# Kernel tuning notes

Measured on AMD Instinct MI355X. Metric: run time of the kernel, lower is better.

Reference implementation:

```python
import jax, jax.numpy as jnp
import numpy as np

H = 8          # num heads
DK = 64        # d_model // H
D_MODEL = 512
WIN = 256


def setup_inputs() -> dict:
    key = jax.random.key(0)
    ks = jax.random.split(key, 12)
    B, S = 2, 2048
    mk = lambda k, shape, s=1.0: jax.random.normal(k, shape, dtype=jnp.float32) * s
    inp = {
        "query": mk(ks[0], (B, S, D_MODEL)),
        "key_in": mk(ks[1], (B, S, D_MODEL)),
        "value": mk(ks[2], (B, S, D_MODEL)),
        # nn.Linear(d_model, d_model) weights (out,in) and biases, x4
        "Wq": mk(ks[3], (D_MODEL, D_MODEL), 0.02), "bq": jnp.zeros((D_MODEL,), jnp.float32),
        "Wk": mk(ks[4], (D_MODEL, D_MODEL), 0.02), "bk": jnp.zeros((D_MODEL,), jnp.float32),
        "Wv": mk(ks[5], (D_MODEL, D_MODEL), 0.02), "bv": jnp.zeros((D_MODEL,), jnp.float32),
        "Wo": mk(ks[6], (D_MODEL, D_MODEL), 0.02), "bo": jnp.zeros((D_MODEL,), jnp.float32),
    }
    return inp


def reference(query, key_in, value, Wq, bq, Wk, bk, Wv, bv, Wo, bo):
    B, S, D = query.shape
    scale = np.float32(1.0 / np.sqrt(DK))

    def proj(x, W, b):
        # (B,S,D) -> (B,H,S,DK)
        return (x @ W.T + b).reshape(B, S, H, DK).transpose(0, 2, 1, 3)

    q = proj(query, Wq, bq)
    k = proj(key_in, Wk, bk)
    v = proj(value, Wv, bv)

    # Faithful to naive_masked_matmul: full (B,H,S,S) scores, with entries
    # OUTSIDE the sliding window left at exactly 0.0 (NOT -inf) before softmax.
    scores = jnp.einsum('bhid,bhjd->bhij', q, k) * scale
    idx = jnp.arange(S)
    band = jnp.abs(idx[:, None] - idx[None, :]) <= (WIN // 2)  # (S,S) bool
    scores = jnp.where(band, scores, jnp.float32(0.0))

    p_attn = jax.nn.softmax(scores, axis=-1)
    x = jnp.einsum('bhij,bhjd->bhid', p_attn, v)          # (B,H,S,DK)
    x = x.transpose(0, 2, 1, 3).reshape(B, S, D)          # (B,S,D)
    return x @ Wo.T + bo
```

## Files before the change

kernel.cpp:

```cpp
#include <hip/hip_runtime.h>
#include <hip/hip_bf16.h>

#define SS 2048
#define DD 512
#define HWIN 128

typedef __bf16 bf16x8 __attribute__((ext_vector_type(8)));
typedef unsigned short u16x8 __attribute__((ext_vector_type(8)));
typedef float f32x4 __attribute__((ext_vector_type(4)));

__device__ __forceinline__ unsigned short f2bf(float x) {
    unsigned u = __builtin_bit_cast(unsigned, x);
    return (unsigned short)((u + 0x7fffu + ((u >> 16) & 1u)) >> 16);
}
__device__ __forceinline__ float bf2f(unsigned short s) {
    unsigned u = ((unsigned)s) << 16;
    return __builtin_bit_cast(float, u);
}
__device__ __forceinline__ void split_bf(float x, unsigned short& h, unsigned short& l) {
    h = f2bf(x);
    l = f2bf(x - bf2f(h));
}
__device__ __forceinline__ void split8(float4 f0, float4 f1, u16x8& h, u16x8& l) {
    const float vals[8] = {f0.x, f0.y, f0.z, f0.w, f1.x, f1.y, f1.z, f1.w};
    #pragma unroll
    for (int i = 0; i < 8; ++i) {
        unsigned short hh, ll;
        split_bf(vals[i], hh, ll);
        h[i] = hh;
        l[i] = ll;
    }
}
__device__ __forceinline__ f32x4 mfma16(u16x8 a, u16x8 b, f32x4 c) {
    return __builtin_amdgcn_mfma_f32_16x16x32_bf16(
        __builtin_bit_cast(bf16x8, a), __builtin_bit_cast(bf16x8, b), c, 0, 0, 0);
}
__device__ __forceinline__ void gload16(const unsigned short* g, unsigned short* l) {
    __builtin_amdgcn_global_load_lds(
        (const __attribute__((address_space(1))) unsigned int*)g,
        (__attribute__((address_space(3))) unsigned int*)l, 16, 0, 0);
}

__global__ __launch_bounds__(256) void castW(
    const float* __restrict__ wq, const float* __restrict__ wk,
    const float* __restrict__ wv, const float* __restrict__ wo,
    unsigned short* __restrict__ WP, unsigned short* __restrict__ WoP)
{
    const size_t e0 = ((size_t)blockIdx.x * 256 + threadIdx.x) * 8;
    const float* src; size_t off; unsigned short* dst;
    if      (e0 < 262144) { src = wq; off = e0;          dst = WP + 2 * e0; }
    else if (e0 < 524288) { src = wk; off = e0 - 262144; dst = WP + 2 * e0; }
    else if (e0 < 786432) { src = wv; off = e0 - 524288; dst = WP + 2 * e0; }
    else                  { src = wo; off = e0 - 786432; dst = WoP + 2 * (e0 - 786432); }
    u16x8 h, l;
    split8(*(const float4*)(src + off), *(const float4*)(src + off + 4), h, l);
    *(u16x8*)(dst)     = h;
    *(u16x8*)(dst + 8) = l;
}

__global__ __launch_bounds__(256) void proj_gemm(
    const float* __restrict__ q, const float* __restrict__ k, const float* __restrict__ v,
    const unsigned short* __restrict__ WP,
    const float* __restrict__ bq, const float* __restrict__ bk, const float* __restrict__ bv,
    unsigned short* __restrict__ base,
    unsigned short* __restrict__ VTH, unsigned short* __restrict__ VTL)
{
    const int d = blockIdx.x;
    const int hi = d >> 6, low = d & 63;
    const int x = low >> 3, rsw = low & 7;
    const int g = hi * 8 + rsw;
    const int y = g / 3, z = g - y * 3;

    const float* A = (z == 0) ? q : ((z == 1) ? k : v);
    const unsigned short* Wp = WP + (size_t)z * 524288;
    const float* bias = (z == 0) ? bq : ((z == 1) ? bk : bv);
    unsigned short* OH = base + (size_t)z * 4194304;

    const int m0 = y * 128, n0 = x * 64;

    __shared__ unsigned short Ah[16 * 64 * 8], Al[16 * 64 * 8];
    __shared__ unsigned short Bh[8 * 64 * 8],  Bl[8 * 64 * 8];

    const int tid = threadIdx.x, wave = tid >> 6, lane = tid & 63;
    const int lm = lane & 15, lq = lane >> 4;
    const int wm = wave >> 1, wn = wave & 1;
    const int kb = lq * 8;

    f32x4 acc[4][2] = {};

    const int ar0 = m0 + (wave * 2 + 0) * 16 + lm;
    const int ar1 = m0 + (wave * 2 + 1) * 16 + lm;
    const int br  = n0 + wave * 16 + lm;

    for (int k0 = 0; k0 < 512; k0 += 64) {
        const float* p0 = A + (size_t)ar0 * 512 + k0 + kb;
        const float* p1 = A + (size_t)ar1 * 512 + k0 + kb;
        const float4 a00 = *(const float4*)(p0),      a01 = *(const float4*)(p0 + 4);
        const float4 a02 = *(const float4*)(p0 + 32), a03 = *(const float4*)(p0 + 36);
        const float4 a10 = *(const float4*)(p1),      a11 = *(const float4*)(p1 + 4);
        const float4 a12 = *(const float4*)(p1 + 32), a13 = *(const float4*)(p1 + 36);

        __syncthreads();
        {
            u16x8 h, l;
            split8(a00, a01, h, l);
            *(u16x8*)&Ah[((0 * 8 + wave * 2 + 0) * 64 + lane) * 8] = h;
            *(u16x8*)&Al[((0 * 8 + wave * 2 + 0) * 64 + lane) * 8] = l;
            split8(a02, a03, h, l);
            *(u16x8*)&Ah[((1 * 8 + wave * 2 + 0) * 64 + lane) * 8] = h;
            *(u16x8*)&Al[((1 * 8 + wave * 2 + 0) * 64 + lane) * 8] = l;
            split8(a10, a11, h, l);
            *(u16x8*)&Ah[((0 * 8 + wave * 2 + 1) * 64 + lane) * 8] = h;
            *(u16x8*)&Al[((0 * 8 + wave * 2 + 1) * 64 + lane) * 8] = l;
            split8(a12, a13, h, l);
            *(u16x8*)&Ah[((1 * 8 + wave * 2 + 1) * 64 + lane) * 8] = h;
            *(u16x8*)&Al[((1 * 8 + wave * 2 + 1) * 64 + lane) * 8] = l;
        }
        {
            const unsigned short* pw0 = Wp + 2 * ((size_t)br * 512 + k0 + kb);
            gload16(pw0,     &Bh[((0 * 4 + wave) * 64 + lane) * 8]);
            gload16(pw0 + 8, &Bl[((0 * 4 + wave) * 64 + lane) * 8]);
            const unsigned short* pw1 = Wp + 2 * ((size_t)br * 512 + k0 + 32 + kb);
            gload16(pw1,     &Bh[((1 * 4 + wave) * 64 + lane) * 8]);
            gload16(pw1 + 8, &Bl[((1 * 4 + wave) * 64 + lane) * 8]);
        }
        __syncthreads();

        #pragma unroll
        for (int s = 0; s < 2; ++s) {
            u16x8 afh[4], afl[4], bfh[2], bfl[2];
            #pragma unroll
            for (int i = 0; i < 4; ++i) {
                afh[i] = *(const u16x8*)&Ah[((s * 8 + wm * 4 + i) * 64 + lane) * 8];
                afl[i] = *(const u16x8*)&Al[((s * 8 + wm * 4 + i) * 64 + lane) * 8];
            }
            #pragma unroll
            for (int j = 0; j < 2; ++j) {
                bfh[j] = *(const u16x8*)&Bh[((s * 4 + wn * 2 + j) * 64 + lane) * 8];
                bfl[j] = *(const u16x8*)&Bl[((s * 4 + wn * 2 + j) * 64 + lane) * 8];
            }
            #pragma unroll
            for (int i = 0; i < 4; ++i)
                #pragma unroll
                for (int j = 0; j < 2; ++j) {
                    acc[i][j] = mfma16(afh[i], bfh[j], acc[i][j]);
                    acc[i][j] = mfma16(afh[i], bfl[j], acc[i][j]);
                    acc[i][j] = mfma16(afl[i], bfh[j], acc[i][j]);
                }
        }
    }

    #pragma unroll
    for (int i = 0; i < 4; ++i)
        #pragma unroll
        for (int j = 0; j < 2; ++j) {
            const int col = n0 + (wn * 2 + j) * 16 + lm;
            const float bv_ = bias[col];
            #pragma unroll
            for (int r = 0; r < 4; ++r) {
                const int row = m0 + (wm * 4 + i) * 16 + lq * 4 + r;
                const float vv = acc[i][j][r] + bv_;
                unsigned short hh, ll;
                split_bf(vv, hh, ll);
                if (z == 2) {
                    const size_t vix =
                        (((size_t)(row >> 11) * 8 + (col >> 6)) * 64 + (col & 63)) * 2048
                        + (row & 2047);
                    VTH[vix] = hh;
                    VTL[vix] = ll;
                } else {
                    OH[(size_t)row * 512 + col] = hh;
                }
            }
        }
}

__global__ __launch_bounds__(256) void out_gemm(
    const unsigned short* __restrict__ XHg, const unsigned short* __restrict__ XLg,
    const unsigned short* __restrict__ WoP, const float* __restrict__ bo,
    float* __restrict__ O)
{
    const int gid = blockIdx.x;
    const int rr = gid & 7, hi = gid >> 3;
    const int nblk = hi & 7, mhi = hi >> 3;
    const int mblk = mhi * 8 + rr;
    const int m0 = mblk * 64, n0 = nblk * 64;

    __shared__ unsigned short Ah[8 * 64 * 8], Al[8 * 64 * 8];
    __shared__ unsigned short Bh[8 * 64 * 8], Bl[8 * 64 * 8];

    const int tid = threadIdx.x, wave = tid >> 6, lane = tid & 63;
    const int lm = lane & 15, lq = lane >> 4;
    const int kb = lq * 8;

    f32x4 acc[4] = {};

    const int arow = m0 + wave * 16 + lm;
    const int brow = n0 + wave * 16 + lm;

    for (int k0 = 0; k0 < 512; k0 += 64) {
        __syncthreads();
        #pragma unroll
        for (int s = 0; s < 2; ++s) {
            gload16(XHg + (size_t)arow * 512 + k0 + s * 32 + kb,
                    &Ah[((s * 4 + wave) * 64 + lane) * 8]);
            gload16(XLg + (size_t)arow * 512 + k0 + s * 32 + kb,
                    &Al[((s * 4 + wave) * 64 + lane) * 8]);
            const unsigned short* pw = WoP + 2 * ((size_t)brow * 512 + k0 + s * 32 + kb);
            gload16(pw,     &Bh[((s * 4 + wave) * 64 + lane) * 8]);
            gload16(pw + 8, &Bl[((s * 4 + wave) * 64 + lane) * 8]);
        }
        __syncthreads();

        #pragma unroll
        for (int s = 0; s < 2; ++s) {
            const u16x8 a_h = *(const u16x8*)&Ah[((s * 4 + wave) * 64 + lane) * 8];
            const u16x8 a_l = *(const u16x8*)&Al[((s * 4 + wave) * 64 + lane) * 8];
            #pragma unroll
            for (int j = 0; j < 4; ++j) {
                const u16x8 b_h = *(const u16x8*)&Bh[((s * 4 + j) * 64 + lane) * 8];
                const u16x8 b_l = *(const u16x8*)&Bl[((s * 4 + j) * 64 + lane) * 8];
                acc[j] = mfma16(a_h, b_h, acc[j]);
                acc[j] = mfma16(a_h, b_l, acc[j]);
                acc[j] = mfma16(a_l, b_h, acc[j]);
            }
        }
    }

    #pragma unroll
    for (int j = 0; j < 4; ++j) {
        const int col = n0 + j * 16 + lm;
        const float bv_ = bo[col];
        #pragma unroll
        for (int r = 0; r < 4; ++r) {
            const int row = m0 + wave * 16 + lq * 4 + r;
            O[(size_t)row * 512 + col] = acc[j][r] + bv_;
        }
    }
}

__global__ __launch_bounds__(256) void vsum_stage1(
    const unsigned short* __restrict__ VTH, const unsigned short* __restrict__ VTL,
    float* __restrict__ partial)
{
    const int bh = blockIdx.x, c = blockIdx.y;
    const int t = threadIdx.x, dd = t & 63, g = t >> 6;
    __shared__ float p[4][64];
    const size_t rb = ((size_t)bh * 64 + dd) * 2048 + c * 64 + g * 16;
    const u16x8 h0 = *(const u16x8*)(VTH + rb), h1 = *(const u16x8*)(VTH + rb + 8);
    const u16x8 l0 = *(const u16x8*)(VTL + rb), l1 = *(const u16x8*)(VTL + rb + 8);
    float acc = 0.f;
    #pragma unroll
    for (int i = 0; i < 8; ++i) acc += bf2f(h0[i]) + bf2f(l0[i]);
    #pragma unroll
    for (int i = 0; i < 8; ++i) acc += bf2f(h1[i]) + bf2f(l1[i]);
    p[g][dd] = acc;
    __syncthreads();
    if (t < 64)
        partial[((size_t)bh * 32 + c) * 64 + t] =
            p[0][t] + p[1][t] + p[2][t] + p[3][t];
}

__global__ __launch_bounds__(64) void vsum_stage2(
    const float* __restrict__ partial, float* __restrict__ VS)
{
    const int bh = blockIdx.x, dd = threadIdx.x;
    float acc = 0.f;
    #pragma unroll 8
    for (int c = 0; c < 32; ++c)
        acc += partial[((size_t)bh * 32 + c) * 64 + dd];
    VS[bh * 64 + dd] = acc;
}

__global__ __launch_bounds__(256) void attn_mfma(
    const unsigned short* __restrict__ QH, const unsigned short* __restrict__ KH,
    const unsigned short* __restrict__ VTH, const float* __restrict__ VS,
    unsigned short* __restrict__ XH, unsigned short* __restrict__ XL)
{
    const int dblk = blockIdx.x;
    const int bhi = dblk >> 8, blow = dblk & 255;
    const int xblk = blow >> 3, rrs = blow & 7;
    const int bh = bhi * 8 + rrs;
    const int h = bh & 7, b = bh >> 3;
    const int i0 = xblk * 64;
    const int tid = threadIdx.x, wave = tid >> 6, lane = tid & 63;
    const int lm = lane & 15, lq = lane >> 4;
    const int kb = lq * 8;

    __shared__ unsigned short KfH[2 * 8 * 64 * 8];
    __shared__ unsigned short VfH[2 * 8 * 64 * 8];
    __shared__ unsigned short Swh[64][72];

    const size_t qoff = ((size_t)(b * SS + i0 + wave * 16 + lm)) * DD + h * 64 + kb;
    const u16x8 aQ0h = *(const u16x8*)(QH + qoff);
    const u16x8 aQ1h = *(const u16x8*)(QH + qoff + 32);

    f32x4 oacc[4] = {};
    float dacc[4] = {0.f, 0.f, 0.f, 0.f};

    const size_t vrow = ((size_t)bh * 64 + wave * 16 + lm) * 2048;
    const int s0 = (wave * 2 + 0) * 64 * 8 + lane * 8;
    const int s1 = (wave * 2 + 1) * 64 * 8 + lane * 8;

    #define STAGE(jt_, bufsel)                                                  \
    {                                                                           \
        const int jt0_ = i0 - 128 + (jt_) * 64;                                 \
        const int jrow = jt0_ + wave * 16 + lm;                                 \
        const int jrc = min(max(jrow, 0), SS - 1);                              \
        const size_t kgb = ((size_t)(b * SS + jrc)) * DD + h * 64 + kb;         \
        gload16(KH + kgb,      &KfH[(bufsel) * 4096 + s0]);                     \
        gload16(KH + kgb + 32, &KfH[(bufsel) * 4096 + s1]);                     \
        const int j0c = min(max(jt0_ + kb, 0), SS - 8);                         \
        const int j1c = min(max(jt0_ + 32 + kb, 0), SS - 8);                    \
        gload16(VTH + vrow + j0c, &VfH[(bufsel) * 4096 + s0]);                  \
        gload16(VTH + vrow + j1c, &VfH[(bufsel) * 4096 + s1]);                  \
    }

    STAGE(0, 0);
    __syncthreads();

    for (int jt = 0; jt < 5; ++jt) {
        const int buf = jt & 1;
        if (jt < 4) STAGE(jt + 1, buf ^ 1);
        const int jt0 = i0 - 128 + jt * 64;

        #pragma unroll
        for (int js = 0; js < 4; ++js) {
            const int j0 = js * 16;
            const u16x8 bK0h = *(const u16x8*)&KfH[buf * 4096 + ((js * 2 + 0) * 64 + lane) * 8];
            const u16x8 bK1h = *(const u16x8*)&KfH[buf * 4096 + ((js * 2 + 1) * 64 + lane) * 8];
            f32x4 s = {0.f, 0.f, 0.f, 0.f};
            s = mfma16(aQ0h, bK0h, s);
            s = mfma16(aQ1h, bK1h, s);
            const int jg = jt0 + j0 + lm;
            const int iq = i0 + wave * 16 + lq * 4;
            #pragma unroll
            for (int r = 0; r < 4; ++r) {
                const int qi = iq + r;
                const bool in = (jg >= 0) && (jg < SS) &&
                                (jg >= qi - HWIN) && (jg <= qi + HWIN);
                const float w = in ? (__expf(s[r] * 0.125f) - 1.0f) : 0.0f;
                dacc[r] += w;
                Swh[wave * 16 + lq * 4 + r][j0 + lm] = f2bf(w);
            }
        }

        const u16x8 aP0h = *(const u16x8*)&Swh[wave * 16 + lm][kb];
        const u16x8 aP1h = *(const u16x8*)&Swh[wave * 16 + lm][kb + 32];
        #pragma unroll
        for (int s4 = 0; s4 < 4; ++s4) {
            const u16x8 bV0h = *(const u16x8*)&VfH[buf * 4096 + ((s4 * 2 + 0) * 64 + lane) * 8];
            const u16x8 bV1h = *(const u16x8*)&VfH[buf * 4096 + ((s4 * 2 + 1) * 64 + lane) * 8];
            oacc[s4] = mfma16(aP0h, bV0h, oacc[s4]);
            oacc[s4] = mfma16(aP1h, bV1h, oacc[s4]);
        }
        __syncthreads();
    }
    #undef STAGE

    #pragma unroll
    for (int r = 0; r < 4; ++r) {
        float v = dacc[r];
        v += __shfl_xor(v, 1);
        v += __shfl_xor(v, 2);
        v += __shfl_xor(v, 4);
        v += __shfl_xor(v, 8);
        dacc[r] = v + 2048.0f;
    }

    #pragma unroll
    for (int s4 = 0; s4 < 4; ++s4) {
        const float vsv = VS[bh * 64 + s4 * 16 + lm];
        #pragma unroll
        for (int r = 0; r < 4; ++r) {
            const int qrow = i0 + wave * 16 + lq * 4 + r;
            const float x = (oacc[s4][r] + vsv) / dacc[r];
            unsigned short xh, xl;
            split_bf(x, xh, xl);
            const size_t ix = ((size_t)(b * SS + qrow)) * DD + h * 64 + s4 * 16 + lm;
            XH[ix] = xh;
            XL[ix] = xl;
        }
    }
}

extern "C" void kernel_launch(void* const* d_in, const int* in_sizes, int n_in,
                              void* d_out, int out_size, void* d_ws, size_t ws_size,
                              hipStream_t stream)
{
    const float* query  = (const float*)d_in[0];
    const float* key_in = (const float*)d_in[1];
    const float* value  = (const float*)d_in[2];
    const float* Wq = (const float*)d_in[3]; const float* bq = (const float*)d_in[4];
    const float* Wk = (const float*)d_in[5]; const float* bk = (const float*)d_in[6];
    const float* Wv = (const float*)d_in[7]; const float* bv = (const float*)d_in[8];
    const float* Wo = (const float*)d_in[9]; const float* bo = (const float*)d_in[10];

    unsigned short* wsb = (unsigned short*)d_ws;
    unsigned short* QH  = wsb;
    unsigned short* KH  = wsb + 4194304;
    unsigned short* VTH = wsb + 8388608;
    unsigned short* VTL = wsb + 10485760;
    unsigned short* XH  = wsb + 12582912;
    unsigned short* XL  = wsb + 14680064;
    unsigned short* WP  = wsb + 16777216;
    unsigned short* WoP = wsb + 18350080;
    float* part = (float*)((char*)d_ws + 62914560);
    float* VSp  = (float*)((char*)d_ws + 63045632);

    castW<<<512, 256, 0, stream>>>(Wq, Wk, Wv, Wo, WP, WoP);

    proj_gemm<<<768, 256, 0, stream>>>(
        query, key_in, value, WP, bq, bk, bv, QH, VTH, VTL);

    vsum_stage1<<<dim3(16, 32), 256, 0, stream>>>(VTH, VTL, part);
    vsum_stage2<<<16, 64, 0, stream>>>(part, VSp);

    attn_mfma<<<512, 256, 0, stream>>>(QH, KH, VTH, VSp, XH, XL);

    out_gemm<<<512, 256, 0, stream>>>(XH, XL, WoP, bo, (float*)d_out);
}
```

Before: 170.8 us.

## Pre-split activations to bf16 pairs and double-buffer LDS in projection GEMMs

The fp32 query/key/value activations are now split into high/low bf16 pairs in a combined cast kernel, alongside the weights. This lets proj_gemm fetch its A tiles with asynchronous global-to-LDS loads instead of loading and splitting them in registers. Both proj_gemm and out_gemm gain a two-stage LDS double buffer, so the next k-slice is prefetched while MFMAs run on the current one, with a single barrier per iteration. The cost is an extra full pass that writes and then re-reads the activation buffers through memory, which adds bandwidth traffic.

```diff
diff --git a/kernel.cpp b/kernel.cpp
--- a/kernel.cpp
+++ b/kernel.cpp
@@ -41,17 +41,27 @@
         (__attribute__((address_space(3))) unsigned int*)l, 16, 0, 0);
 }
 
-__global__ __launch_bounds__(256) void castW(
+__global__ __launch_bounds__(256) void castAll(
+    const float* __restrict__ q, const float* __restrict__ k, const float* __restrict__ v,
     const float* __restrict__ wq, const float* __restrict__ wk,
     const float* __restrict__ wv, const float* __restrict__ wo,
+    unsigned short* __restrict__ AP,
     unsigned short* __restrict__ WP, unsigned short* __restrict__ WoP)
 {
     const size_t e0 = ((size_t)blockIdx.x * 256 + threadIdx.x) * 8;
     const float* src; size_t off; unsigned short* dst;
-    if      (e0 < 262144) { src = wq; off = e0;          dst = WP + 2 * e0; }
-    else if (e0 < 524288) { src = wk; off = e0 - 262144; dst = WP + 2 * e0; }
-    else if (e0 < 786432) { src = wv; off = e0 - 524288; dst = WP + 2 * e0; }
-    else                  { src = wo; off = e0 - 786432; dst = WoP + 2 * (e0 - 786432); }
+    if (e0 < 6291456) {
+        const size_t z = e0 >> 21;
+        off = e0 - (z << 21);
+        src = (z == 0) ? q : ((z == 1) ? k : v);
+        dst = AP + z * 4194304 + 2 * off;
+    } else {
+        const size_t e = e0 - 6291456;
+        if      (e < 262144) { src = wq; off = e;          dst = WP + 2 * e; }
+        else if (e < 524288) { src = wk; off = e - 262144; dst = WP + 2 * e; }
+        else if (e < 786432) { src = wv; off = e - 524288; dst = WP + 2 * e; }
+        else                 { src = wo; off = e - 786432; dst = WoP + 2 * (e - 786432); }
+    }
     u16x8 h, l;
     split8(*(const float4*)(src + off), *(const float4*)(src + off + 4), h, l);
     *(u16x8*)(dst)     = h;
@@ -59,7 +69,7 @@
 }
 
 __global__ __launch_bounds__(256) void proj_gemm(
-    const float* __restrict__ q, const float* __restrict__ k, const float* __restrict__ v,
+    const unsigned short* __restrict__ AP,
     const unsigned short* __restrict__ WP,
     const float* __restrict__ bq, const float* __restrict__ bk, const float* __restrict__ bv,
     unsigned short* __restrict__ base,
@@ -71,15 +81,15 @@
     const int g = hi * 8 + rsw;
     const int y = g / 3, z = g - y * 3;
 
-    const float* A = (z == 0) ? q : ((z == 1) ? k : v);
-    const unsigned short* Wp = WP + (size_t)z * 524288;
+    const unsigned short* APz = AP + (size_t)z * 4194304;
+    const unsigned short* Wp  = WP + (size_t)z * 524288;
     const float* bias = (z == 0) ? bq : ((z == 1) ? bk : bv);
     unsigned short* OH = base + (size_t)z * 4194304;
 
     const int m0 = y * 128, n0 = x * 64;
 
-    __shared__ unsigned short Ah[16 * 64 * 8], Al[16 * 64 * 8];
-    __shared__ unsigned short Bh[8 * 64 * 8],  Bl[8 * 64 * 8];
+    __shared__ unsigned short Ah[2 * 4096], Al[2 * 4096];
+    __shared__ unsigned short Bh[2 * 2048], Bl[2 * 2048];
 
     const int tid = threadIdx.x, wave = tid >> 6, lane = tid & 63;
     const int lm = lane & 15, lq = lane >> 4;
@@ -92,63 +102,53 @@
     const int ar1 = m0 + (wave * 2 + 1) * 16 + lm;
     const int br  = n0 + wave * 16 + lm;
 
-    for (int k0 = 0; k0 < 512; k0 += 64) {
-        const float* p0 = A + (size_t)ar0 * 512 + k0 + kb;
-        const float* p1 = A + (size_t)ar1 * 512 + k0 + kb;
-        const float4 a00 = *(const float4*)(p0),      a01 = *(const float4*)(p0 + 4);
-        const float4 a02 = *(const float4*)(p0 + 32), a03 = *(const float4*)(p0 + 36);
-        const float4 a10 = *(const float4*)(p1),      a11 = *(const float4*)(p1 + 4);
-        const float4 a12 = *(const float4*)(p1 + 32), a13 = *(const float4*)(p1 + 36);
-
-        __syncthreads();
-        {
-            u16x8 h, l;
-            split8(a00, a01, h, l);
-            *(u16x8*)&Ah[((0 * 8 + wave * 2 + 0) * 64 + lane) * 8] = h;
-            *(u16x8*)&Al[((0 * 8 + wave * 2 + 0) * 64 + lane) * 8] = l;
-            split8(a02, a03, h, l);
-            *(u16x8*)&Ah[((1 * 8 + wave * 2 + 0) * 64 + lane) * 8] = h;
-            *(u16x8*)&Al[((1 * 8 + wave * 2 + 0) * 64 + lane) * 8] = l;
-            split8(a10, a11, h, l);
-            *(u16x8*)&Ah[((0 * 8 + wave * 2 + 1) * 64 + lane) * 8] = h;
-            *(u16x8*)&Al[((0 * 8 + wave * 2 + 1) * 64 + lane) * 8] = l;
-            split8(a12, a13, h, l);
-            *(u16x8*)&Ah[((1 * 8 + wave * 2 + 1) * 64 + lane) * 8] = h;
-            *(u16x8*)&Al[((1 * 8 + wave * 2 + 1) * 64 + lane) * 8] = l;
-        }
-        {
-            const unsigned short* pw0 = Wp + 2 * ((size_t)br * 512 + k0 + kb);
-            gload16(pw0,     &Bh[((0 * 4 + wave) * 64 + lane) * 8]);
-            gload16(pw0 + 8, &Bl[((0 * 4 + wave) * 64 + lane) * 8]);
-            const unsigned short* pw1 = Wp + 2 * ((size_t)br * 512 + k0 + 32 + kb);
-            gload16(pw1,     &Bh[((1 * 4 + wave) * 64 + lane) * 8]);
-            gload16(pw1 + 8, &Bl[((1 * 4 + wave) * 64 + lane) * 8]);
-        }
-        __syncthreads();
-
-        #pragma unroll
-        for (int s = 0; s < 2; ++s) {
-            u16x8 afh[4], afl[4], bfh[2], bfl[2];
-            #pragma unroll
-            for (int i = 0; i < 4; ++i) {
-                afh[i] = *(const u16x8*)&Ah[((s * 8 + wm * 4 + i) * 64 + lane) * 8];
-                afl[i] = *(const u16x8*)&Al[((s * 8 + wm * 4 + i) * 64 + lane) * 8];
-            }
+    const int aoff0 = ((wave * 2 + 0) * 64 + lane) * 8;
+    const int aoff1 = ((wave * 2 + 1) * 64 + lane) * 8;
+    const int boff  = (wave * 64 + lane) * 8;
+
+    #define PSTAGE(k0_, bs)                                                     \
+    {                                                                           \
+        const unsigned short* pa0 = APz + 2 * ((size_t)ar0 * 512 + (k0_) + kb); \
+        gload16(pa0,     &Ah[(bs) * 4096 + aoff0]);                             \
+        gload16(pa0 + 8, &Al[(bs) * 4096 + aoff0]);                             \
+        const unsigned short* pa1 = APz + 2 * ((size_t)ar1 * 512 + (k0_) + kb); \
+        gload16(pa1,     &Ah[(bs) * 4096 + aoff1]);                             \
+        gload16(pa1 + 8, &Al[(bs) * 4096 + aoff1]);                             \
+        const unsigned short* pw = Wp + 2 * ((size_t)br * 512 + (k0_) + kb);    \
+        gload16(pw,     &Bh[(bs) * 2048 + boff]);                               \
+        gload16(pw + 8, &Bl[(bs) * 2048 + boff]);                               \
+    }
+
+    PSTAGE(0, 0);
+    __syncthreads();
+
+    for (int t = 0; t < 16; ++t) {
+        const int cur = t & 1;
+        if (t < 15) PSTAGE((t + 1) * 32, cur ^ 1);
+
+        u16x8 afh[4], afl[4], bfh[2], bfl[2];
+        #pragma unroll
+        for (int i = 0; i < 4; ++i) {
+            afh[i] = *(const u16x8*)&Ah[cur * 4096 + ((wm * 4 + i) * 64 + lane) * 8];
+            afl[i] = *(const u16x8*)&Al[cur * 4096 + ((wm * 4 + i) * 64 + lane) * 8];
+        }
+        #pragma unroll
+        for (int j = 0; j < 2; ++j) {
+            bfh[j] = *(const u16x8*)&Bh[cur * 2048 + ((wn * 2 + j) * 64 + lane) * 8];
+            bfl[j] = *(const u16x8*)&Bl[cur * 2048 + ((wn * 2 + j) * 64 + lane) * 8];
+        }
+        #pragma unroll
+        for (int i = 0; i < 4; ++i)
             #pragma unroll
             for (int j = 0; j < 2; ++j) {
-                bfh[j] = *(const u16x8*)&Bh[((s * 4 + wn * 2 + j) * 64 + lane) * 8];
-                bfl[j] = *(const u16x8*)&Bl[((s * 4 + wn * 2 + j) * 64 + lane) * 8];
+                acc[i][j] = mfma16(afh[i], bfh[j], acc[i][j]);
+                acc[i][j] = mfma16(afh[i], bfl[j], acc[i][j]);
+                acc[i][j] = mfma16(afl[i], bfh[j], acc[i][j]);
             }
-            #pragma unroll
-            for (int i = 0; i < 4; ++i)
-                #pragma unroll
-                for (int j = 0; j < 2; ++j) {
-                    acc[i][j] = mfma16(afh[i], bfh[j], acc[i][j]);
-                    acc[i][j] = mfma16(afh[i], bfl[j], acc[i][j]);
-                    acc[i][j] = mfma16(afl[i], bfh[j], acc[i][j]);
-                }
-        }
-    }
+
+        __syncthreads();
+    }
+    #undef PSTAGE
 
     #pragma unroll
     for (int i = 0; i < 4; ++i)
@@ -186,8 +186,8 @@
     const int mblk = mhi * 8 + rr;
     const int m0 = mblk * 64, n0 = nblk * 64;
 
-    __shared__ unsigned short Ah[8 * 64 * 8], Al[8 * 64 * 8];
-    __shared__ unsigned short Bh[8 * 64 * 8], Bl[8 * 64 * 8];
+    __shared__ unsigned short Ah[2 * 4096], Al[2 * 4096];
+    __shared__ unsigned short Bh[2 * 4096], Bl[2 * 4096];
 
     const int tid = threadIdx.x, wave = tid >> 6, lane = tid & 63;
     const int lm = lane & 15, lq = lane >> 4;
@@ -198,34 +198,44 @@
     const int arow = m0 + wave * 16 + lm;
     const int brow = n0 + wave * 16 + lm;
 
-    for (int k0 = 0; k0 < 512; k0 += 64) {
-        __syncthreads();
+    #define OSTAGE(k0_, bs)                                                     \
+    {                                                                           \
+        _Pragma("unroll")                                                       \
+        for (int s = 0; s < 2; ++s) {                                           \
+            const int o = (bs) * 4096 + ((s * 4 + wave) * 64 + lane) * 8;       \
+            gload16(XHg + (size_t)arow * 512 + (k0_) + s * 32 + kb, &Ah[o]);    \
+            gload16(XLg + (size_t)arow * 512 + (k0_) + s * 32 + kb, &Al[o]);    \
+            const unsigned short* pw =                                          \
+                WoP + 2 * ((size_t)brow * 512 + (k0_) + s * 32 + kb);           \
+            gload16(pw,     &Bh[o]);                                            \
+            gload16(pw + 8, &Bl[o]);                                            \
+        }                                                                       \
+    }
+
+    OSTAGE(0, 0);
+    __syncthreads();
+
+    for (int t = 0; t < 8; ++t) {
+        const int cur = t & 1;
+        if (t < 7) OSTAGE((t + 1) * 64, cur ^ 1);
+
         #pragma unroll
         for (int s = 0; s < 2; ++s) {
-            gload16(XHg + (size_t)arow * 512 + k0 + s * 32 + kb,
-                    &Ah[((s * 4 + wave) * 64 + lane) * 8]);
-            gload16(XLg + (size_t)arow * 512 + k0 + s * 32 + kb,
-                    &Al[((s * 4 + wave) * 64 + lane) * 8]);
-            const unsigned short* pw = WoP + 2 * ((size_t)brow * 512 + k0 + s * 32 + kb);
-            gload16(pw,     &Bh[((s * 4 + wave) * 64 + lane) * 8]);
-            gload16(pw + 8, &Bl[((s * 4 + wave) * 64 + lane) * 8]);
-        }
-        __syncthreads();
-
-        #pragma unroll
-        for (int s = 0; s < 2; ++s) {
-            const u16x8 a_h = *(const u16x8*)&Ah[((s * 4 + wave) * 64 + lane) * 8];
-            const u16x8 a_l = *(const u16x8*)&Al[((s * 4 + wave) * 64 + lane) * 8];
+            const u16x8 a_h = *(const u16x8*)&Ah[cur * 4096 + ((s * 4 + wave) * 64 + lane) * 8];
+            const u16x8 a_l = *(const u16x8*)&Al[cur * 4096 + ((s * 4 + wave) * 64 + lane) * 8];
             #pragma unroll
             for (int j = 0; j < 4; ++j) {
-                const u16x8 b_h = *(const u16x8*)&Bh[((s * 4 + j) * 64 + lane) * 8];
-                const u16x8 b_l = *(const u16x8*)&Bl[((s * 4 + j) * 64 + lane) * 8];
+                const u16x8 b_h = *(const u16x8*)&Bh[cur * 4096 + ((s * 4 + j) * 64 + lane) * 8];
+                const u16x8 b_l = *(const u16x8*)&Bl[cur * 4096 + ((s * 4 + j) * 64 + lane) * 8];
                 acc[j] = mfma16(a_h, b_h, acc[j]);
                 acc[j] = mfma16(a_h, b_l, acc[j]);
                 acc[j] = mfma16(a_l, b_h, acc[j]);
             }
         }
-    }
+
+        __syncthreads();
+    }
+    #undef OSTAGE
 
     #pragma unroll
     for (int j = 0; j < 4; ++j) {
@@ -405,13 +415,14 @@
     unsigned short* XL  = wsb + 14680064;
     unsigned short* WP  = wsb + 16777216;
     unsigned short* WoP = wsb + 18350080;
+    unsigned short* AP  = wsb + 18874368;
     float* part = (float*)((char*)d_ws + 62914560);
     float* VSp  = (float*)((char*)d_ws + 63045632);
 
-    castW<<<512, 256, 0, stream>>>(Wq, Wk, Wv, Wo, WP, WoP);
-
-    proj_gemm<<<768, 256, 0, stream>>>(
-        query, key_in, value, WP, bq, bk, bv, QH, VTH, VTL);
+    castAll<<<3584, 256, 0, stream>>>(query, key_in, value, Wq, Wk, Wv, Wo,
+                                      AP, WP, WoP);
+
+    proj_gemm<<<768, 256, 0, stream>>>(AP, WP, bq, bk, bv, QH, VTH, VTL);
 
     vsum_stage1<<<dim3(16, 32), 256, 0, stream>>>(VTH, VTL, part);
     vsum_stage2<<<16, 64, 0, stream>>>(part, VSp);
```

New measurement: 181.9 us. 1.07x slower.
